# Kernel tuning notes

Measured on AMD Instinct MI355X. Metric: run time of the kernel, lower is better.

## Reference

```python
import jax, jax.numpy as jnp
import numpy as np

B, T_PLUS_2, H, K = 128, 2050, 64, 100
BETA = 1.0


def setup_inputs() -> dict:
    key = jax.random.key(0)
    ks = jax.random.split(key, 7)
    event_tensor = jax.random.randint(ks[0], (B, T_PLUS_2), 0, K)            # fine event types
    dtime_tensor = jax.random.uniform(ks[1], (B, T_PLUS_2), dtype=jnp.float32)
    scale = 1.0 / np.sqrt(H)
    in_emb = jax.random.normal(ks[2], (K + 3, H), dtype=jnp.float32) * scale  # +BOS/EOS/PAD rows
    Wx = jax.random.normal(ks[3], (H, 7 * H), dtype=jnp.float32) * scale      # input -> 7 gates
    Wh = jax.random.normal(ks[4], (H, 7 * H), dtype=jnp.float32) * scale      # hidden -> 7 gates
    b = jnp.zeros((7 * H,), dtype=jnp.float32)
    out_emb = jax.random.normal(ks[5], (K, H), dtype=jnp.float32) * scale     # coarse-type embeddings
    return {"event_tensor": event_tensor, "dtime_tensor": dtime_tensor,
            "in_emb": in_emb, "Wx": Wx, "Wh": Wh, "b": b, "out_emb": out_emb}


def _ctlstm_intensities(event_tensor, dtime_tensor, in_emb, Wx, Wh, b, out_emb):
    # Embed input events for steps 0..T (drop last token): [B, T+1, H]
    emb = in_emb[event_tensor[:, :-1]]
    # Precompute the input-dependent part of all 7 gates outside the scan.
    pre = jnp.einsum('bth,hg->btg', emb, Wx) + b        # [B, T+1, 7H]
    dt = dtime_tensor[:, 1:]                            # [B, T+1] dtime to next event

    batch = event_tensor.shape[0]
    h_dim = in_emb.shape[1]
    init = (jnp.zeros((batch, h_dim), jnp.float32),     # c(t_i-)
            jnp.zeros((batch, h_dim), jnp.float32),     # cell_bar
            jnp.zeros((batch, h_dim), jnp.float32))     # h(t_i-)

    def step(carry, inp):
        c_minus, cb_prev, h_minus = carry
        pre_t, dt_t = inp                               # [B,7H], [B]
        g = pre_t + h_minus @ Wh
        gi, gf, gz, go, gib, gfb, gd = jnp.split(g, 7, axis=-1)
        i = jax.nn.sigmoid(gi)
        f = jax.nn.sigmoid(gf)
        z = jnp.tanh(gz)
        o = jax.nn.sigmoid(go)
        i_bar = jax.nn.sigmoid(gib)
        f_bar = jax.nn.sigmoid(gfb)
        delta = jax.nn.softplus(gd)
        c_i = f * c_minus + i * z
        cb_i = f_bar * cb_prev + i_bar * z
        # decay over the interval dt: c(t)=cb+(c-cb)exp(-delta dt), h=o*tanh(c)
        c_next = cb_i + (c_i - cb_i) * jnp.exp(-delta * dt_t[:, None])
        h_next = o * jnp.tanh(c_next)
        return (c_next, cb_i, h_next), h_next

    _, hs = jax.lax.scan(step, init, (pre.transpose(1, 0, 2), dt.T))
    hs = hs.transpose(1, 0, 2)                          # [B, T+1, H] hidden at t_{i+1}^-
    # softplus with beta: (1/beta) * softplus(beta * x); identity fine<->coarse map
    logits = jnp.einsum('bth,kh->btk', hs, out_emb)
    return jax.nn.softplus(BETA * logits) / BETA        # [B, T+1, K]


def reference(event_tensor, dtime_tensor, in_emb, Wx, Wh, b, out_emb):
    return _ctlstm_intensities(event_tensor, dtime_tensor, in_emb, Wx, Wh, b, out_emb)
```

## Files before the change

### kernel.cpp

```cpp
#include <hip/hip_runtime.h>
#include <math.h>

#define BB 128
#define T2 2050
#define TT 2049
#define HH 64
#define GG 448
#define KK 100
#define NE 103
#define TCHUNK 128
#define NCHUNK 17

#define LOG2E 1.44269504088896340736f
#define LN2   0.69314718055994530942f

__device__ __forceinline__ float frcp(float x) { return __builtin_amdgcn_rcpf(x); }

__device__ __forceinline__ float sigmoid_fast(float x) {
    return frcp(1.f + exp2f(-x * LOG2E));
}
__device__ __forceinline__ float tanh_fast(float x) {
    float e = exp2f(x * (2.f * LOG2E));
    return 1.f - 2.f * frcp(1.f + e);
}
__device__ __forceinline__ float softplus_fast(float x) {
    float t = exp2f(-fabsf(x) * LOG2E);
    return fmaxf(x, 0.f) + LN2 * log2f(1.f + t);
}
__device__ __forceinline__ float expn_fast(float x) {
    return exp2f(x * LOG2E);
}

__global__ void pre_emb_kernel(const float* __restrict__ in_emb,
                               const float* __restrict__ Wx,
                               const float* __restrict__ bias,
                               float* __restrict__ pre_emb) {
    int e = blockIdx.x;
    int t = threadIdx.x;
    float acc = bias[t];
#pragma unroll
    for (int k = 0; k < HH; ++k)
        acc = fmaf(in_emb[e * HH + k], Wx[k * GG + t], acc);
    pre_emb[e * GG + t] = acc;
}

__device__ __forceinline__ float dot64(const float* __restrict__ hs,
                                       const float* __restrict__ w) {
    const float4* h4 = (const float4*)hs;
    float a0 = 0.f, a1 = 0.f, a2 = 0.f, a3 = 0.f;
#pragma unroll
    for (int k4 = 0; k4 < HH / 4; ++k4) {
        float4 hv = h4[k4];
        a0 = fmaf(hv.x, w[4 * k4 + 0], a0);
        a1 = fmaf(hv.y, w[4 * k4 + 1], a1);
        a2 = fmaf(hv.z, w[4 * k4 + 2], a2);
        a3 = fmaf(hv.w, w[4 * k4 + 3], a3);
    }
    return (a0 + a1) + (a2 + a3);
}

__launch_bounds__(GG, 1)
__global__ void scan_kernel(const int* __restrict__ event,
                            const float* __restrict__ dtime,
                            const float* __restrict__ pre_emb,
                            const float* __restrict__ Wh,
                            float* __restrict__ out) {
    const int b    = blockIdx.x;
    const int tid  = threadIdx.x;
    const int w    = tid >> 6;
    const int lane = tid & 63;

    __shared__ __align__(16) float gbuf[2][GG];
    __shared__ __align__(16) float h_sw[7][HH];

    float wcol[HH];
#pragma unroll
    for (int k = 0; k < HH; ++k) wcol[k] = Wh[k * GG + tid];

    const int*   ev_row  = event + b * T2;
    const float* dt_row  = dtime + b * T2;
    float*       out_row = out + (size_t)b * TT * KK;

    {
        int   ev0 = ev_row[0];
        float pe0 = pre_emb[ev0 * GG + tid];
        float dt0 = dt_row[1];
        float v0;
        if (w == 2)      v0 = tanh_fast(pe0);
        else if (w == 6) v0 = expn_fast(-softplus_fast(pe0) * dt0);
        else             v0 = sigmoid_fast(pe0);
        gbuf[0][tid] = v0;
    }

    float pe_cur = pre_emb[ev_row[1] * GG + tid];
    int   evn    = ev_row[2];
    float dt_cur = dt_row[2];

    float c = 0.f, cb = 0.f;
    __syncthreads();

    for (int t = 0; t < TT; ++t) {
        const bool more = (t < TT - 1);
        float pe_nxt = 0.f, dt_new = 0.f;
        int   ev_new = 0;
        if (more) {
            pe_nxt = pre_emb[evn * GG + tid];
            int tn = (t + 3 < T2) ? (t + 3) : (T2 - 1);
            ev_new = ev_row[tn];
            dt_new = dt_row[tn];
        }

        const float* gb = gbuf[t & 1];
        const float gi  = gb[lane];
        const float gf  = gb[HH + lane];
        const float gz  = gb[2 * HH + lane];
        const float go  = gb[3 * HH + lane];
        const float gib = gb[4 * HH + lane];
        const float gfb = gb[5 * HH + lane];
        const float ed  = gb[6 * HH + lane];
        const float ci  = fmaf(gf, c, gi * gz);
        const float cbi = fmaf(gfb, cb, gib * gz);
        const float cn  = fmaf(ci - cbi, ed, cbi);
        const float h   = go * tanh_fast(cn);
        c  = cn;
        cb = cbi;

        if (tid < HH) out_row[(size_t)t * KK + tid] = h;

        h_sw[w][lane] = h;

        if (more) {
            float acc = pe_cur + dot64(h_sw[w], wcol);
            float val;
            if (w == 2)      val = tanh_fast(acc);
            else if (w == 6) val = expn_fast(-softplus_fast(acc) * dt_cur);
            else             val = sigmoid_fast(acc);
            gbuf[(t + 1) & 1][tid] = val;
            pe_cur = pe_nxt;
            evn    = ev_new;
            dt_cur = dt_new;
        }
        __syncthreads();
    }
}

__launch_bounds__(128)
__global__ void logits_kernel(const float* __restrict__ oe,
                              float* __restrict__ out) {
    const int b   = blockIdx.x;
    const int t0  = blockIdx.y * TCHUNK;
    const int nt  = (TT - t0 < TCHUNK) ? (TT - t0) : TCHUNK;
    const int tid = threadIdx.x;

    __shared__ __align__(16) float hs[TCHUNK][HH];

    float* row = out + ((size_t)b * TT + t0) * KK;

    const int n4 = nt * (HH / 4);
    for (int i4 = tid; i4 < n4; i4 += 128) {
        int tt = i4 >> 4, q = i4 & 15;
        ((float4*)&hs[tt][0])[q] = ((const float4*)(row + (size_t)tt * KK))[q];
    }

    float wk[HH];
    if (tid < KK) {
#pragma unroll
        for (int q = 0; q < HH / 4; ++q)
            ((float4*)wk)[q] = ((const float4*)(oe + tid * HH))[q];
    }
    __syncthreads();

    if (tid < KK) {
        for (int tt = 0; tt < nt; ++tt) {
            float lg = dot64(&hs[tt][0], wk);
            row[(size_t)tt * KK + tid] = softplus_fast(lg);
        }
    }
}

extern "C" void kernel_launch(void* const* d_in, const int* in_sizes, int n_in,
                              void* d_out, int out_size, void* d_ws, size_t ws_size,
                              hipStream_t stream) {
    const int*   event  = (const int*)d_in[0];
    const float* dtime  = (const float*)d_in[1];
    const float* in_emb = (const float*)d_in[2];
    const float* Wx     = (const float*)d_in[3];
    const float* Wh     = (const float*)d_in[4];
    const float* bias   = (const float*)d_in[5];
    const float* oe     = (const float*)d_in[6];
    float*       out    = (float*)d_out;

    float* pre_emb = (float*)d_ws;

    pre_emb_kernel<<<NE, GG, 0, stream>>>(in_emb, Wx, bias, pre_emb);
    scan_kernel<<<BB, GG, 0, stream>>>(event, dtime, pre_emb, Wh, out);
    logits_kernel<<<dim3(BB, NCHUNK), 128, 0, stream>>>(oe, out);
}
```

Before: 1.661 ms.

## Use split-bf16 MFMA for recurrent matvec and rework logits kernel

```diff
diff --git a/kernel.cpp b/kernel.cpp
--- a/kernel.cpp
+++ b/kernel.cpp
@@ -14,6 +14,9 @@
 #define LOG2E 1.44269504088896340736f
 #define LN2   0.69314718055994530942f
 
+typedef short bf16x8 __attribute__((ext_vector_type(8)));
+typedef float f32x4  __attribute__((ext_vector_type(4)));
+
 __device__ __forceinline__ float frcp(float x) { return __builtin_amdgcn_rcpf(x); }
 
 __device__ __forceinline__ float sigmoid_fast(float x) {
@@ -29,6 +32,16 @@
 }
 __device__ __forceinline__ float expn_fast(float x) {
     return exp2f(x * LOG2E);
+}
+
+__device__ __forceinline__ unsigned short bf16_rne(float f) {
+    unsigned int u = __builtin_bit_cast(unsigned int, f);
+    unsigned int r = u + 0x7FFFu + ((u >> 16) & 1u);
+    return (unsigned short)(r >> 16);
+}
+__device__ __forceinline__ float bf16_to_f(unsigned short s) {
+    unsigned int u = ((unsigned int)s) << 16;
+    return __builtin_bit_cast(float, u);
 }
 
 __global__ void pre_emb_kernel(const float* __restrict__ in_emb,
@@ -44,137 +57,163 @@
     pre_emb[e * GG + t] = acc;
 }
 
-__device__ __forceinline__ float dot64(const float* __restrict__ hs,
-                                       const float* __restrict__ w) {
-    const float4* h4 = (const float4*)hs;
-    float a0 = 0.f, a1 = 0.f, a2 = 0.f, a3 = 0.f;
-#pragma unroll
-    for (int k4 = 0; k4 < HH / 4; ++k4) {
-        float4 hv = h4[k4];
-        a0 = fmaf(hv.x, w[4 * k4 + 0], a0);
-        a1 = fmaf(hv.y, w[4 * k4 + 1], a1);
-        a2 = fmaf(hv.z, w[4 * k4 + 2], a2);
-        a3 = fmaf(hv.w, w[4 * k4 + 3], a3);
-    }
-    return (a0 + a1) + (a2 + a3);
-}
-
-__launch_bounds__(GG, 1)
+__launch_bounds__(256, 1)
 __global__ void scan_kernel(const int* __restrict__ event,
                             const float* __restrict__ dtime,
                             const float* __restrict__ pre_emb,
                             const float* __restrict__ Wh,
                             float* __restrict__ out) {
-    const int b    = blockIdx.x;
-    const int tid  = threadIdx.x;
-    const int w    = tid >> 6;
-    const int lane = tid & 63;
-
-    __shared__ __align__(16) float gbuf[2][GG];
-    __shared__ __align__(16) float h_sw[7][HH];
-
-    float wcol[HH];
-#pragma unroll
-    for (int k = 0; k < HH; ++k) wcol[k] = Wh[k * GG + tid];
+    const int b   = blockIdx.x;
+    const int tid = threadIdx.x;
+    const int w   = tid >> 6;
+    const int l   = tid & 63;
+    const int q   = l >> 4;
+    const int m   = l & 15;
+    const int e   = (w << 4) | m;
+
+    __shared__ __align__(16) unsigned short hs_hi[2][HH];
+    __shared__ __align__(16) unsigned short hs_lo[2][HH];
+
+    bf16x8 Bhi[7][2], Blo[7][2];
+#pragma unroll
+    for (int g = 0; g < 7; ++g) {
+#pragma unroll
+        for (int kh = 0; kh < 2; ++kh) {
+            const int col = g * 64 + e;
+            bf16x8 bh, bl;
+#pragma unroll
+            for (int j = 0; j < 8; ++j) {
+                const int k = kh * 32 + q * 8 + j;
+                const float v = Wh[k * GG + col];
+                const unsigned short hi = bf16_rne(v);
+                const float lof = v - bf16_to_f(hi);
+                bh[j] = (short)hi;
+                bl[j] = (short)bf16_rne(lof);
+            }
+            Bhi[g][kh] = bh;
+            Blo[g][kh] = bl;
+        }
+    }
+
+    if (tid < HH) { hs_hi[0][tid] = 0; hs_lo[0][tid] = 0; }
 
     const int*   ev_row  = event + b * T2;
     const float* dt_row  = dtime + b * T2;
     float*       out_row = out + (size_t)b * TT * KK;
 
+    float pre_cur[7], pre_nxt[7];
     {
-        int   ev0 = ev_row[0];
-        float pe0 = pre_emb[ev0 * GG + tid];
-        float dt0 = dt_row[1];
-        float v0;
-        if (w == 2)      v0 = tanh_fast(pe0);
-        else if (w == 6) v0 = expn_fast(-softplus_fast(pe0) * dt0);
-        else             v0 = sigmoid_fast(pe0);
-        gbuf[0][tid] = v0;
-    }
-
-    float pe_cur = pre_emb[ev_row[1] * GG + tid];
-    int   evn    = ev_row[2];
-    float dt_cur = dt_row[2];
+        const int ev0 = ev_row[0];
+#pragma unroll
+        for (int g = 0; g < 7; ++g) pre_cur[g] = pre_emb[ev0 * GG + g * 64 + e];
+    }
+    int   evn    = ev_row[1];
+    float dt_cur = dt_row[1];
 
     float c = 0.f, cb = 0.f;
     __syncthreads();
 
     for (int t = 0; t < TT; ++t) {
-        const bool more = (t < TT - 1);
-        float pe_nxt = 0.f, dt_new = 0.f;
-        int   ev_new = 0;
-        if (more) {
-            pe_nxt = pre_emb[evn * GG + tid];
-            int tn = (t + 3 < T2) ? (t + 3) : (T2 - 1);
-            ev_new = ev_row[tn];
-            dt_new = dt_row[tn];
-        }
-
-        const float* gb = gbuf[t & 1];
-        const float gi  = gb[lane];
-        const float gf  = gb[HH + lane];
-        const float gz  = gb[2 * HH + lane];
-        const float go  = gb[3 * HH + lane];
-        const float gib = gb[4 * HH + lane];
-        const float gfb = gb[5 * HH + lane];
-        const float ed  = gb[6 * HH + lane];
-        const float ci  = fmaf(gf, c, gi * gz);
-        const float cbi = fmaf(gfb, cb, gib * gz);
+#pragma unroll
+        for (int g = 0; g < 7; ++g) pre_nxt[g] = pre_emb[evn * GG + g * 64 + e];
+        int t2 = t + 2; if (t2 > T2 - 1) t2 = T2 - 1;
+        const int   ev_new = ev_row[t2];
+        const float dt_nxt = dt_row[t2];
+
+        const int rb = t & 1;
+        const bf16x8 Ahi0 = *(const bf16x8*)&hs_hi[rb][q * 8];
+        const bf16x8 Ahi1 = *(const bf16x8*)&hs_hi[rb][32 + q * 8];
+        const bf16x8 Alo0 = *(const bf16x8*)&hs_lo[rb][q * 8];
+        const bf16x8 Alo1 = *(const bf16x8*)&hs_lo[rb][32 + q * 8];
+
+        float gate[7];
+#pragma unroll
+        for (int g = 0; g < 7; ++g) {
+            const float p = pre_cur[g];
+            f32x4 accA = { p, p, p, p };
+            f32x4 accB = { 0.f, 0.f, 0.f, 0.f };
+            accA = __builtin_amdgcn_mfma_f32_16x16x32_bf16(Ahi0, Bhi[g][0], accA, 0, 0, 0);
+            accB = __builtin_amdgcn_mfma_f32_16x16x32_bf16(Ahi1, Bhi[g][1], accB, 0, 0, 0);
+            accA = __builtin_amdgcn_mfma_f32_16x16x32_bf16(Alo0, Bhi[g][0], accA, 0, 0, 0);
+            accB = __builtin_amdgcn_mfma_f32_16x16x32_bf16(Alo1, Bhi[g][1], accB, 0, 0, 0);
+            accA = __builtin_amdgcn_mfma_f32_16x16x32_bf16(Ahi0, Blo[g][0], accA, 0, 0, 0);
+            accB = __builtin_amdgcn_mfma_f32_16x16x32_bf16(Ahi1, Blo[g][1], accB, 0, 0, 0);
+            gate[g] = accA[0] + accB[0];
+        }
+
+        const float i_g  = sigmoid_fast(gate[0]);
+        const float f_g  = sigmoid_fast(gate[1]);
+        const float z_g  = tanh_fast(gate[2]);
+        const float o_g  = sigmoid_fast(gate[3]);
+        const float ib_g = sigmoid_fast(gate[4]);
+        const float fb_g = sigmoid_fast(gate[5]);
+        const float ed   = expn_fast(-softplus_fast(gate[6]) * dt_cur);
+
+        const float ci  = fmaf(f_g, c, i_g * z_g);
+        const float cbi = fmaf(fb_g, cb, ib_g * z_g);
         const float cn  = fmaf(ci - cbi, ed, cbi);
-        const float h   = go * tanh_fast(cn);
+        const float h   = o_g * tanh_fast(cn);
         c  = cn;
         cb = cbi;
 
-        if (tid < HH) out_row[(size_t)t * KK + tid] = h;
-
-        h_sw[w][lane] = h;
-
-        if (more) {
-            float acc = pe_cur + dot64(h_sw[w], wcol);
-            float val;
-            if (w == 2)      val = tanh_fast(acc);
-            else if (w == 6) val = expn_fast(-softplus_fast(acc) * dt_cur);
-            else             val = sigmoid_fast(acc);
-            gbuf[(t + 1) & 1][tid] = val;
-            pe_cur = pe_nxt;
-            evn    = ev_new;
-            dt_cur = dt_new;
-        }
+        const unsigned short hhi = bf16_rne(h);
+        const float          hre = h - bf16_to_f(hhi);
+        const unsigned short hlo = bf16_rne(hre);
+        const int wbuf = (t + 1) & 1;
+        if (l < 16) {
+            hs_hi[wbuf][e] = hhi;
+            hs_lo[wbuf][e] = hlo;
+            out_row[(size_t)t * KK + e] = h;
+        }
+
+#pragma unroll
+        for (int g = 0; g < 7; ++g) pre_cur[g] = pre_nxt[g];
+        evn    = ev_new;
+        dt_cur = dt_nxt;
         __syncthreads();
     }
 }
 
-__launch_bounds__(128)
+__launch_bounds__(256)
 __global__ void logits_kernel(const float* __restrict__ oe,
                               float* __restrict__ out) {
-    const int b   = blockIdx.x;
-    const int t0  = blockIdx.y * TCHUNK;
-    const int nt  = (TT - t0 < TCHUNK) ? (TT - t0) : TCHUNK;
-    const int tid = threadIdx.x;
-
-    __shared__ __align__(16) float hs[TCHUNK][HH];
-
-    float* row = out + ((size_t)b * TT + t0) * KK;
-
-    const int n4 = nt * (HH / 4);
-    for (int i4 = tid; i4 < n4; i4 += 128) {
-        int tt = i4 >> 4, q = i4 & 15;
-        ((float4*)&hs[tt][0])[q] = ((const float4*)(row + (size_t)tt * KK))[q];
-    }
-
-    float wk[HH];
-    if (tid < KK) {
-#pragma unroll
-        for (int q = 0; q < HH / 4; ++q)
-            ((float4*)wk)[q] = ((const float4*)(oe + tid * HH))[q];
-    }
-    __syncthreads();
-
-    if (tid < KK) {
-        for (int tt = 0; tt < nt; ++tt) {
-            float lg = dot64(&hs[tt][0], wk);
-            row[(size_t)tt * KK + tid] = softplus_fast(lg);
-        }
+    const int b    = blockIdx.x;
+    const int t0   = blockIdx.y * TCHUNK;
+    const int nt   = (TT - t0 < TCHUNK) ? (TT - t0) : TCHUNK;
+    const int tid  = threadIdx.x;
+    const int wv   = tid >> 6;
+    const int lane = tid & 63;
+
+    const int  c1     = (lane < KK - HH) ? (HH + lane) : (KK - 1);
+    const bool has_c1 = (lane < KK - HH);
+
+    float wk0[HH], wk1[HH];
+#pragma unroll
+    for (int qq = 0; qq < HH / 4; ++qq) {
+        ((float4*)wk0)[qq] = ((const float4*)(oe + lane * HH))[qq];
+        ((float4*)wk1)[qq] = ((const float4*)(oe + c1 * HH))[qq];
+    }
+
+    for (int tt = wv; tt < nt; tt += 4) {
+        float* row = out + ((size_t)b * TT + t0 + tt) * KK;
+        float a0 = 0.f, a1 = 0.f, a2 = 0.f, a3 = 0.f;
+        float b0 = 0.f, b1 = 0.f, b2 = 0.f, b3 = 0.f;
+#pragma unroll
+        for (int qq = 0; qq < HH / 4; ++qq) {
+            const float4 hv = ((const float4*)row)[qq];
+            a0 = fmaf(hv.x, wk0[4 * qq + 0], a0);
+            a1 = fmaf(hv.y, wk0[4 * qq + 1], a1);
+            a2 = fmaf(hv.z, wk0[4 * qq + 2], a2);
+            a3 = fmaf(hv.w, wk0[4 * qq + 3], a3);
+            b0 = fmaf(hv.x, wk1[4 * qq + 0], b0);
+            b1 = fmaf(hv.y, wk1[4 * qq + 1], b1);
+            b2 = fmaf(hv.z, wk1[4 * qq + 2], b2);
+            b3 = fmaf(hv.w, wk1[4 * qq + 3], b3);
+        }
+        const float lg0 = (a0 + a1) + (a2 + a3);
+        const float lg1 = (b0 + b1) + (b2 + b3);
+        row[lane] = softplus_fast(lg0);
+        if (has_c1) row[HH + lane] = softplus_fast(lg1);
     }
 }
 
@@ -193,6 +232,6 @@
     float* pre_emb = (float*)d_ws;
 
     pre_emb_kernel<<<NE, GG, 0, stream>>>(in_emb, Wx, bias, pre_emb);
-    scan_kernel<<<BB, GG, 0, stream>>>(event, dtime, pre_emb, Wh, out);
-    logits_kernel<<<dim3(BB, NCHUNK), 128, 0, stream>>>(oe, out);
-}
+    scan_kernel<<<BB, 256, 0, stream>>>(event, dtime, pre_emb, Wh, out);
+    logits_kernel<<<dim3(BB, NCHUNK), 256, 0, stream>>>(oe, out);
+}
```

Result: slower. 1.904 ms (+14.6%).
